# Kernel tuning notes

Hardware: AMD Instinct MI355X
Metric: run time of the kernel (lower is better)

The kernel has to match this reference:

```python
import jax, jax.numpy as jnp
import numpy as np

N = 50000
E = 800000
D = 512
H = 256
K = 16
COLLAPSE_REG = 1.0


def setup_inputs() -> dict:
    key = jax.random.key(0)
    ks = jax.random.split(key, 8)
    embeddings = jax.random.normal(ks[0], (N, D), dtype=jnp.float32)
    edge_src = jax.random.randint(ks[1], (E,), 0, N, dtype=jnp.int32)
    edge_dst = jax.random.randint(ks[2], (E,), 0, N, dtype=jnp.int32)
    # GCNConv params (glorot-ish scaling)
    W1 = jax.random.normal(ks[3], (D, H), dtype=jnp.float32) / np.sqrt(D)
    b1 = jnp.zeros((H,), dtype=jnp.float32)
    W2 = jax.random.normal(ks[4], (H, H), dtype=jnp.float32) / np.sqrt(H)
    b2 = jnp.zeros((H,), dtype=jnp.float32)
    Wa = jax.random.normal(ks[5], (H, K), dtype=jnp.float32) / np.sqrt(H)
    ba = jnp.zeros((K,), dtype=jnp.float32)
    return {"embeddings": embeddings, "edge_src": edge_src, "edge_dst": edge_dst,
            "W1": W1, "b1": b1, "W2": W2, "b2": b2, "Wa": Wa, "ba": ba}


def _gcn_conv(x, W, b, src, dst, dis):
    # PyG GCNConv: transform then D^{-1/2}(A+I)D^{-1/2} aggregation + bias.
    x = x @ W                                   # [N, out]
    norm = dis[src] * dis[dst]                  # [E]
    agg = jax.ops.segment_sum(x[src] * norm[:, None], dst, num_segments=N)
    agg = agg + (dis * dis)[:, None] * x        # self-loop term
    return agg + b


def reference(embeddings, edge_src, edge_dst, W1, b1, W2, b2, Wa, ba):
    # symmetric-norm degrees with self-loops (edge weight 1)
    deg = 1.0 + jax.ops.segment_sum(jnp.ones((E,), jnp.float32), edge_dst, num_segments=N)
    dis = jax.lax.rsqrt(deg)                    # deg > 0 always (self-loop)

    x = jax.nn.selu(_gcn_conv(embeddings, W1, b1, edge_src, edge_dst, dis))
    x_skip = x  # dropout is identity in eval
    x = jax.nn.selu(_gcn_conv(x, W2, b2, edge_src, edge_dst, dis))
    x = x + x_skip
    assignments = jax.nn.softmax(x @ Wa + ba, axis=1)   # [N, K]

    # ---- DMoN losses (faithful to original, incl. scalar normalizer) ----
    degrees = jax.ops.segment_sum(jnp.ones((E,), jnp.float32), edge_src, num_segments=N)  # row sums of A
    m = degrees.sum() / 2.0
    AS = jax.ops.segment_sum(assignments[edge_dst], edge_src, num_segments=N)  # A @ S, [N, K]
    trace_pooled = jnp.sum(assignments * AS)    # trace(S^T A S)
    dS = degrees @ assignments                  # [K]
    normalizer = jnp.dot(dS, dS) / (2.0 * m)    # scalar (as in original code)
    spectral_loss = -(trace_pooled - K * normalizer) / (2.0 * m)

    cluster_sizes = assignments.sum(axis=0)     # [K]
    collapse_loss = jnp.linalg.norm(cluster_sizes) / N * jnp.sqrt(jnp.float32(K)) - 1.0
    entropy = -jnp.sum(assignments * jnp.log(assignments + 1e-8)) / N
    entropy_loss = -0.1 * entropy
    total_loss = spectral_loss + COLLAPSE_REG * collapse_loss + entropy_loss

    pooled = (assignments / (cluster_sizes + 1e-8)).T @ embeddings  # [K, D]
    return (assignments, pooled, spectral_loss, COLLAPSE_REG * collapse_loss, total_loss, entropy_loss)
```

## Files before the change

kernel.cpp:

```cpp
#include <hip/hip_runtime.h>
#include <hip/hip_fp16.h>
#include <math.h>

#define NN 50000
#define EE 800000
#define DD 512
#define HH 256
#define KK 16
#define NB_SCAN 196

typedef _Float16 half8_t __attribute__((ext_vector_type(8)));
typedef float f32x4 __attribute__((ext_vector_type(4)));

__global__ void zero_kernel(int* __restrict__ p, int n) {
    int i = blockIdx.x * blockDim.x + threadIdx.x;
    if (i < n) p[i] = 0;
}

__global__ void count_kernel(const int4* __restrict__ src4, const int4* __restrict__ dst4,
                             int* __restrict__ indeg, int* __restrict__ outdeg) {
    int e = blockIdx.x * blockDim.x + threadIdx.x;
    if (e < EE / 4) {
        int4 s = src4[e], d = dst4[e];
        atomicAdd(&outdeg[s.x], 1); atomicAdd(&outdeg[s.y], 1);
        atomicAdd(&outdeg[s.z], 1); atomicAdd(&outdeg[s.w], 1);
        atomicAdd(&indeg[d.x], 1);  atomicAdd(&indeg[d.y], 1);
        atomicAdd(&indeg[d.z], 1);  atomicAdd(&indeg[d.w], 1);
    }
}

__global__ void scan_p1(const int* __restrict__ in, int* __restrict__ part, int n,
                        const int* __restrict__ outdeg, float* __restrict__ dis,
                        float* __restrict__ degf) {
    __shared__ int tile[256];
    int t = threadIdx.x;
    int i = blockIdx.x * 256 + t;
    int v = (i < n) ? in[i] : 0;
    tile[t] = v;
    if (i < n) {
        dis[i]  = 1.0f / sqrtf(1.0f + (float)v);
        degf[i] = (float)outdeg[i];
    }
    __syncthreads();
    for (int o = 128; o > 0; o >>= 1) {
        if (t < o) tile[t] += tile[t + o];
        __syncthreads();
    }
    if (t == 0) part[blockIdx.x] = tile[0];
}

__global__ void scan_p2(int* __restrict__ part, int nb, int* __restrict__ off_end) {
    __shared__ int tile[256];
    int t = threadIdx.x;
    int v = (t < nb) ? part[t] : 0;
    tile[t] = v;
    __syncthreads();
    for (int o = 1; o < 256; o <<= 1) {
        int x = (t >= o) ? tile[t - o] : 0;
        __syncthreads();
        tile[t] += x;
        __syncthreads();
    }
    if (t < nb) part[t] = tile[t] - v;
    if (t == 255) *off_end = tile[255];
}

__global__ void scan_p3(const int* __restrict__ in, const int* __restrict__ part,
                        int* __restrict__ out, int n) {
    __shared__ int tile[256];
    int t = threadIdx.x;
    int i = blockIdx.x * 256 + t;
    int v = (i < n) ? in[i] : 0;
    tile[t] = v;
    __syncthreads();
    for (int o = 1; o < 256; o <<= 1) {
        int x = (t >= o) ? tile[t - o] : 0;
        __syncthreads();
        tile[t] += x;
        __syncthreads();
    }
    if (i < n) out[i] = part[blockIdx.x] + tile[t] - v;
}

__global__ void scatter_kernel(const int4* __restrict__ src4, const int4* __restrict__ dst4,
                               const int* __restrict__ off, int* __restrict__ cur,
                               int* __restrict__ nbr) {
    int e = blockIdx.x * blockDim.x + threadIdx.x;
    if (e < EE / 4) {
        int4 s = src4[e], d = dst4[e];
        int p;
        p = atomicAdd(&cur[d.x], 1); nbr[off[d.x] + p] = s.x;
        p = atomicAdd(&cur[d.y], 1); nbr[off[d.y] + p] = s.y;
        p = atomicAdd(&cur[d.z], 1); nbr[off[d.z] + p] = s.z;
        p = atomicAdd(&cur[d.w], 1); nbr[off[d.w] + p] = s.w;
    }
}

__global__ void transpose_w(const float* __restrict__ W1, __half* __restrict__ Wt1,
                            const float* __restrict__ W2, __half* __restrict__ Wt2,
                            const float* __restrict__ Wa, __half* __restrict__ WaT) {
    int i = blockIdx.x * 256 + threadIdx.x;
    if (i < DD * HH) {
        int k = i / HH, n = i % HH;
        Wt1[(size_t)n * DD + k] = __float2half(W1[i]);
    } else if (i < DD * HH + HH * HH) {
        int j = i - DD * HH;
        int k = j / HH, n = j % HH;
        Wt2[(size_t)n * HH + k] = __float2half(W2[j]);
    } else if (i < DD * HH + HH * HH + HH * KK) {
        int j = i - DD * HH - HH * HH;
        int k = j / KK, n = j % KK;
        WaT[n * HH + k] = __float2half(Wa[j]);
    }
}

template <typename TA, int KDIM>
__global__ __launch_bounds__(256) void mfma_gemm(const TA* __restrict__ A,
                                                 const __half* __restrict__ Bt,
                                                 __half* __restrict__ C, int M) {
    constexpr bool F32 = sizeof(TA) == 4;
    constexpr int SROW = F32 ? 36 : 40;
    constexpr int EPG  = F32 ? 4 : 8;
    constexpr int GPR  = 32 / EPG;
    constexpr int RPP  = 256 / GPR;
    constexpr int NP   = 128 / RPP;
    constexpr int KI   = KDIM / 32;

    __shared__ TA As[2][128 * SROW];

    int t = threadIdx.x;
    int wave = t >> 6, lane = t & 63, quad = lane >> 4, l16 = lane & 15;
    int row0 = blockIdx.x * 128, col0 = blockIdx.y * 128;
    int wm = (wave & 1) * 64, wn = (wave >> 1) * 64;
    int srow = t / GPR, sg = t % GPR;

    f32x4 acc[4][4] = {};
    uint4 sreg[NP];
    uint4 bcur[4];

    const __half* brow[4];
#pragma unroll
    for (int ni = 0; ni < 4; ni++)
        brow[ni] = Bt + (size_t)(col0 + wn + ni * 16 + l16) * KDIM + quad * 8;

    auto gloadA = [&](int k0) {
#pragma unroll
        for (int p = 0; p < NP; p++) {
            int gr = row0 + p * RPP + srow;
            if (gr < M)
                sreg[p] = *(const uint4*)(A + (size_t)gr * KDIM + k0 + sg * EPG);
            else
                sreg[p] = make_uint4(0, 0, 0, 0);
        }
    };
    auto sstore = [&](int buf) {
#pragma unroll
        for (int p = 0; p < NP; p++)
            *(uint4*)&As[buf][(p * RPP + srow) * SROW + sg * EPG] = sreg[p];
    };

    gloadA(0);
#pragma unroll
    for (int ni = 0; ni < 4; ni++) bcur[ni] = *(const uint4*)(brow[ni]);
    sstore(0);
    __syncthreads();

#pragma unroll
    for (int i = 0; i < KI; i++) {
        int cur = i & 1;
        uint4 bnext[4];
        if (i + 1 < KI) {
            gloadA((i + 1) * 32);
#pragma unroll
            for (int ni = 0; ni < 4; ni++)
                bnext[ni] = *(const uint4*)(brow[ni] + (i + 1) * 32);
        }

        half8_t af[4];
#pragma unroll
        for (int mi = 0; mi < 4; mi++) {
            int row = wm + mi * 16 + l16;
            if constexpr (F32) {
                const float* pl = (const float*)&As[cur][0] + row * SROW + quad * 8;
                float4 x0 = *(const float4*)pl;
                float4 x1 = *(const float4*)(pl + 4);
                half8_t h;
                h[0] = (_Float16)x0.x; h[1] = (_Float16)x0.y;
                h[2] = (_Float16)x0.z; h[3] = (_Float16)x0.w;
                h[4] = (_Float16)x1.x; h[5] = (_Float16)x1.y;
                h[6] = (_Float16)x1.z; h[7] = (_Float16)x1.w;
                af[mi] = h;
            } else {
                af[mi] = *(const half8_t*)&As[cur][row * SROW + quad * 8];
            }
        }
#pragma unroll
        for (int mi = 0; mi < 4; mi++)
#pragma unroll
            for (int ni = 0; ni < 4; ni++)
                acc[mi][ni] = __builtin_amdgcn_mfma_f32_16x16x32_f16(
                    af[mi], *(half8_t*)&bcur[ni], acc[mi][ni], 0, 0, 0);

        if (i + 1 < KI) {
            sstore(cur ^ 1);
#pragma unroll
            for (int ni = 0; ni < 4; ni++) bcur[ni] = bnext[ni];
        }
        __syncthreads();
    }

#pragma unroll
    for (int mi = 0; mi < 4; mi++) {
#pragma unroll
        for (int r = 0; r < 4; r++) {
            int rr = row0 + wm + mi * 16 + quad * 4 + r;
            if (rr < M) {
#pragma unroll
                for (int ni = 0; ni < 4; ni++) {
                    C[(size_t)rr * HH + col0 + wn + ni * 16 + l16] =
                        __float2half(acc[mi][ni][r]);
                }
            }
        }
    }
}

__device__ inline void fma8(float* acc, uint4 raw, float w) {
    const __half2* h = (const __half2*)&raw;
#pragma unroll
    for (int i = 0; i < 4; i++) {
        float2 f = __half22float2(h[i]);
        acc[2 * i]     += w * f.x;
        acc[2 * i + 1] += w * f.y;
    }
}

__global__ __launch_bounds__(256) void agg_selu(const __half* __restrict__ T,
                                                const float* __restrict__ dis,
                                                const int* __restrict__ off,
                                                const int* __restrict__ nbr,
                                                const float* __restrict__ bias,
                                                const __half* skip, __half* out) {
    int t = threadIdx.x;
    int l32 = t & 31;
    int n = blockIdx.x * 8 + (t >> 5);
    int c = l32 * 8;
    float dn = dis[n];

    float acc[8];
#pragma unroll
    for (int i = 0; i < 8; i++) acc[i] = 0.f;
    fma8(acc, *(const uint4*)(T + (size_t)n * HH + c), dn * dn);

    int s0 = off[n], s1 = off[n + 1];
    for (int base = s0; base < s1; base += 32) {
        int cnt = min(32, s1 - base);
        int sidv = 0; float sdsv = 0.f;
        if (l32 < cnt) {
            sidv = nbr[base + l32];
            sdsv = dis[sidv] * dn;
        }
        int j = 0;
        for (; j + 8 <= cnt; j += 8) {
            int a0 = __shfl(sidv, j, 32),     a1 = __shfl(sidv, j + 1, 32);
            int a2 = __shfl(sidv, j + 2, 32), a3 = __shfl(sidv, j + 3, 32);
            int a4 = __shfl(sidv, j + 4, 32), a5 = __shfl(sidv, j + 5, 32);
            int a6 = __shfl(sidv, j + 6, 32), a7 = __shfl(sidv, j + 7, 32);
            float w0 = __shfl(sdsv, j, 32),     w1 = __shfl(sdsv, j + 1, 32);
            float w2 = __shfl(sdsv, j + 2, 32), w3 = __shfl(sdsv, j + 3, 32);
            float w4 = __shfl(sdsv, j + 4, 32), w5 = __shfl(sdsv, j + 5, 32);
            float w6 = __shfl(sdsv, j + 6, 32), w7 = __shfl(sdsv, j + 7, 32);
            uint4 r0 = *(const uint4*)(T + (size_t)a0 * HH + c);
            uint4 r1 = *(const uint4*)(T + (size_t)a1 * HH + c);
            uint4 r2 = *(const uint4*)(T + (size_t)a2 * HH + c);
            uint4 r3 = *(const uint4*)(T + (size_t)a3 * HH + c);
            uint4 r4 = *(const uint4*)(T + (size_t)a4 * HH + c);
            uint4 r5 = *(const uint4*)(T + (size_t)a5 * HH + c);
            uint4 r6 = *(const uint4*)(T + (size_t)a6 * HH + c);
            uint4 r7 = *(const uint4*)(T + (size_t)a7 * HH + c);
            fma8(acc, r0, w0); fma8(acc, r1, w1);
            fma8(acc, r2, w2); fma8(acc, r3, w3);
            fma8(acc, r4, w4); fma8(acc, r5, w5);
            fma8(acc, r6, w6); fma8(acc, r7, w7);
        }
        for (; j < cnt; j++) {
            int s = __shfl(sidv, j, 32);
            float w = __shfl(sdsv, j, 32);
            fma8(acc, *(const uint4*)(T + (size_t)s * HH + c), w);
        }
    }

    const float scale = 1.0507009873554805f;
    const float alpha = 1.6732632423543772f;
    float4 b0 = *(const float4*)(bias + c);
    float4 b1 = *(const float4*)(bias + c + 4);
    float bb[8] = {b0.x, b0.y, b0.z, b0.w, b1.x, b1.y, b1.z, b1.w};
    float sk8[8];
#pragma unroll
    for (int i = 0; i < 8; i++) sk8[i] = 0.f;
    if (skip) {
        uint4 raw = *(const uint4*)(skip + (size_t)n * HH + c);
        const __half2* h = (const __half2*)&raw;
#pragma unroll
        for (int i = 0; i < 4; i++) {
            float2 f = __half22float2(h[i]);
            sk8[2 * i] = f.x; sk8[2 * i + 1] = f.y;
        }
    }
    _Float16 res[8];
#pragma unroll
    for (int i = 0; i < 8; i++) {
        float v = acc[i] + bb[i];
        float r = v > 0.f ? scale * v : scale * alpha * expm1f(v);
        res[i] = (_Float16)(r + sk8[i]);
    }
    *(uint4*)(out + (size_t)n * HH + c) = *(uint4*)res;
}

__global__ __launch_bounds__(256) void assign_mfma(const __half* __restrict__ Hb,
                                                   const __half* __restrict__ WaT,
                                                   const float* __restrict__ ba,
                                                   const float* __restrict__ degf,
                                                   float* __restrict__ out_assign,
                                                   __half* __restrict__ out_f16,
                                                   float* __restrict__ scal) {
    int t = threadIdx.x;
    int wave = t >> 6, lane = t & 63, quad = lane >> 4, l16 = lane & 15;
    int nb = blockIdx.x * 256 + wave * 64;

    f32x4 acc[4] = {};
    const __half* bp = WaT + l16 * HH + quad * 8;
    const __half* ap[4];
#pragma unroll
    for (int mi = 0; mi < 4; mi++) {
        int r = nb + mi * 16 + l16;
        if (r >= NN) r = NN - 1;
        ap[mi] = Hb + (size_t)r * HH + quad * 8;
    }
#pragma unroll
    for (int s = 0; s < 8; s++) {
        half8_t bf = *(const half8_t*)(bp + s * 32);
#pragma unroll
        for (int mi = 0; mi < 4; mi++) {
            half8_t af = *(const half8_t*)(ap[mi] + s * 32);
            acc[mi] = __builtin_amdgcn_mfma_f32_16x16x32_f16(af, bf, acc[mi], 0, 0, 0);
        }
    }

    float myb = ba[l16];
    float lcs = 0.f, ldS = 0.f, lent = 0.f;
#pragma unroll
    for (int mi = 0; mi < 4; mi++) {
#pragma unroll
        for (int r = 0; r < 4; r++) {
            int node = nb + mi * 16 + quad * 4 + r;
            bool ok = node < NN;
            float logit = acc[mi][r] + myb;
            float mx = logit;
            for (int o = 1; o < 16; o <<= 1) mx = fmaxf(mx, __shfl_xor(mx, o, 16));
            float e = expf(logit - mx);
            float sum = e;
            for (int o = 1; o < 16; o <<= 1) sum += __shfl_xor(sum, o, 16);
            float a = e / sum;
            if (ok) {
                out_assign[(size_t)node * KK + l16] = a;
                out_f16[(size_t)node * KK + l16] = __float2half(a);
                lcs += a;
                ldS += degf[node] * a;
                lent += a * logf(a + 1e-8f);
            }
        }
    }
    lcs += __shfl_xor(lcs, 16); lcs += __shfl_xor(lcs, 32);
    ldS += __shfl_xor(ldS, 16); ldS += __shfl_xor(ldS, 32);
    for (int o = 32; o >= 1; o >>= 1) lent += __shfl_xor(lent, o);
    if (quad == 0) {
        atomicAdd(&scal[l16], lcs);
        atomicAdd(&scal[16 + l16], ldS);
    }
    if (lane == 0) atomicAdd(&scal[33], lent);
}

__device__ inline float dot16h(const __half* a, const __half* b) {
    uint4 a0 = *(const uint4*)a, a1 = *(const uint4*)(a + 8);
    uint4 b0 = *(const uint4*)b, b1 = *(const uint4*)(b + 8);
    float p = 0.f;
    const __half2* xa = (const __half2*)&a0;
    const __half2* xb = (const __half2*)&b0;
#pragma unroll
    for (int i = 0; i < 4; i++) {
        float2 u = __half22float2(xa[i]), v = __half22float2(xb[i]);
        p += u.x * v.x + u.y * v.y;
    }
    xa = (const __half2*)&a1; xb = (const __half2*)&b1;
#pragma unroll
    for (int i = 0; i < 4; i++) {
        float2 u = __half22float2(xa[i]), v = __half22float2(xb[i]);
        p += u.x * v.x + u.y * v.y;
    }
    return p;
}

__global__ __launch_bounds__(256) void edge_trace(const int4* __restrict__ src4,
                                                  const int4* __restrict__ dst4,
                                                  const __half* __restrict__ Ah,
                                                  float* __restrict__ scal) {
    int e = blockIdx.x * blockDim.x + threadIdx.x;
    float p = 0.f;
    if (e < EE / 4) {
        int4 s = src4[e], d = dst4[e];
        p += dot16h(Ah + (size_t)s.x * KK, Ah + (size_t)d.x * KK);
        p += dot16h(Ah + (size_t)s.y * KK, Ah + (size_t)d.y * KK);
        p += dot16h(Ah + (size_t)s.z * KK, Ah + (size_t)d.z * KK);
        p += dot16h(Ah + (size_t)s.w * KK, Ah + (size_t)d.w * KK);
    }
    for (int o = 32; o >= 1; o >>= 1) p += __shfl_xor(p, o);
    __shared__ float sp;
    if (threadIdx.x == 0) sp = 0.f;
    __syncthreads();
    if ((threadIdx.x & 63) == 0) atomicAdd(&sp, p);
    __syncthreads();
    if (threadIdx.x == 0) atomicAdd(&scal[32], sp);
}

#define PCH 125
__global__ __launch_bounds__(256) void pooled_partial(const float* __restrict__ emb,
                                                      const float* __restrict__ assign,
                                                      float* __restrict__ pool_acc) {
    int d = blockIdx.x * 256 + threadIdx.x;
    int c0 = blockIdx.y * PCH;
    float acc[KK];
#pragma unroll
    for (int k = 0; k < KK; k++) acc[k] = 0.f;
    __shared__ float sa[PCH * KK];
    {
        const float4* srcv = (const float4*)(assign + (size_t)c0 * KK);
        float4* dstv = (float4*)sa;
        for (int i = threadIdx.x; i < PCH * KK / 4; i += 256) dstv[i] = srcv[i];
    }
    __syncthreads();
    for (int j = 0; j < PCH; j++) {
        float ev = emb[(size_t)(c0 + j) * DD + d];
#pragma unroll
        for (int k4 = 0; k4 < 4; k4++) {
            float4 s4 = *(const float4*)&sa[j * KK + k4 * 4];
            acc[k4 * 4 + 0] += s4.x * ev;
            acc[k4 * 4 + 1] += s4.y * ev;
            acc[k4 * 4 + 2] += s4.z * ev;
            acc[k4 * 4 + 3] += s4.w * ev;
        }
    }
#pragma unroll
    for (int k = 0; k < KK; k++) atomicAdd(&pool_acc[k * DD + d], acc[k]);
}

__global__ void finalize(const float* __restrict__ pool_acc, const float* __restrict__ scal,
                         float* __restrict__ out) {
    int bx = blockIdx.x, t = threadIdx.x;
    if (bx < 32) {
        int i = bx * 256 + t;
        int k = i / DD;
        out[800000 + i] = pool_acc[i] / (scal[k] + 1e-8f);
    } else if (t == 0) {
        float cs2 = 0.f, ds2 = 0.f;
        for (int k = 0; k < KK; k++) {
            cs2 += scal[k] * scal[k];
            ds2 += scal[16 + k] * scal[16 + k];
        }
        float two_m = (float)EE;
        float normalizer = ds2 / two_m;
        float trace = scal[32];
        float spectral = -(trace - (float)KK * normalizer) / two_m;
        float collapse = sqrtf(cs2) / (float)NN * 4.0f - 1.0f;
        float entl = 0.1f * scal[33] / (float)NN;
        out[808192] = spectral;
        out[808193] = collapse;
        out[808194] = spectral + collapse + entl;
        out[808195] = entl;
    }
}

extern "C" void kernel_launch(void* const* d_in, const int* in_sizes, int n_in,
                              void* d_out, int out_size, void* d_ws, size_t ws_size,
                              hipStream_t stream) {
    const float* emb = (const float*)d_in[0];
    const int* esrc  = (const int*)d_in[1];
    const int* edst  = (const int*)d_in[2];
    const float* W1  = (const float*)d_in[3];
    const float* b1  = (const float*)d_in[4];
    const float* W2  = (const float*)d_in[5];
    const float* b2  = (const float*)d_in[6];
    const float* Wa  = (const float*)d_in[7];
    const float* ba  = (const float*)d_in[8];
    float* out = (float*)d_out;

    int* indeg      = (int*)d_ws;
    int* outdeg     = indeg + 50000;
    int* cur        = outdeg + 50000;
    float* pool_acc = (float*)(cur + 50000);
    float* scal     = pool_acc + 8192;
    int* part       = (int*)(scal + 64);
    int* off        = part + 256;
    int* nbr        = off + 50004;
    float* dis      = (float*)(nbr + 800000);
    float* degf     = dis + 50000;
    __half* Wt1     = (__half*)(degf + 50000);
    __half* Wt2     = Wt1 + 256 * 512;
    __half* WaT     = Wt2 + 256 * 256;
    __half* T       = WaT + 16 * 256;
    __half* Hb      = T + (size_t)NN * HH;
    __half* Ah      = T;

    zero_kernel<<<dim3(619), 256, 0, stream>>>((int*)d_ws, 158256);
    count_kernel<<<dim3(782), 256, 0, stream>>>((const int4*)esrc, (const int4*)edst,
                                                indeg, outdeg);

    scan_p1<<<dim3(NB_SCAN), 256, 0, stream>>>(indeg, part, NN, outdeg, dis, degf);
    scan_p2<<<dim3(1), 256, 0, stream>>>(part, NB_SCAN, off + NN);
    scan_p3<<<dim3(NB_SCAN), 256, 0, stream>>>(indeg, part, off, NN);
    scatter_kernel<<<dim3(782), 256, 0, stream>>>((const int4*)esrc, (const int4*)edst,
                                                  off, cur, nbr);

    transpose_w<<<dim3(784), 256, 0, stream>>>(W1, Wt1, W2, Wt2, Wa, WaT);

    mfma_gemm<float, DD><<<dim3(392, 2), 256, 0, stream>>>(emb, Wt1, T, NN);
    agg_selu<<<dim3(6250), 256, 0, stream>>>(T, dis, off, nbr, b1, nullptr, Hb);

    mfma_gemm<__half, HH><<<dim3(392, 2), 256, 0, stream>>>(Hb, Wt2, T, NN);
    agg_selu<<<dim3(6250), 256, 0, stream>>>(T, dis, off, nbr, b2, Hb, Hb);

    assign_mfma<<<dim3(196), 256, 0, stream>>>(Hb, WaT, ba, degf, out, Ah, scal);
    edge_trace<<<dim3(782), 256, 0, stream>>>((const int4*)esrc, (const int4*)edst, Ah, scal);
    pooled_partial<<<dim3(2, 400), 256, 0, stream>>>(emb, out, pool_acc);
    finalize<<<dim3(33), 256, 0, stream>>>(pool_acc, scal, out);
}
```

Measured before the change: 563.8 us.

## Slice GEMM output into column panels and precompute edge weights for aggregation

```diff
diff --git a/kernel.cpp b/kernel.cpp
--- a/kernel.cpp
+++ b/kernel.cpp
@@ -84,15 +84,20 @@
 
 __global__ void scatter_kernel(const int4* __restrict__ src4, const int4* __restrict__ dst4,
                                const int* __restrict__ off, int* __restrict__ cur,
-                               int* __restrict__ nbr) {
+                               const float* __restrict__ dis,
+                               int* __restrict__ nbr, __half* __restrict__ wgt) {
     int e = blockIdx.x * blockDim.x + threadIdx.x;
     if (e < EE / 4) {
         int4 s = src4[e], d = dst4[e];
-        int p;
-        p = atomicAdd(&cur[d.x], 1); nbr[off[d.x] + p] = s.x;
-        p = atomicAdd(&cur[d.y], 1); nbr[off[d.y] + p] = s.y;
-        p = atomicAdd(&cur[d.z], 1); nbr[off[d.z] + p] = s.z;
-        p = atomicAdd(&cur[d.w], 1); nbr[off[d.w] + p] = s.w;
+        int p, q;
+        p = atomicAdd(&cur[d.x], 1); q = off[d.x] + p;
+        nbr[q] = s.x; wgt[q] = __float2half(dis[s.x] * dis[d.x]);
+        p = atomicAdd(&cur[d.y], 1); q = off[d.y] + p;
+        nbr[q] = s.y; wgt[q] = __float2half(dis[s.y] * dis[d.y]);
+        p = atomicAdd(&cur[d.z], 1); q = off[d.z] + p;
+        nbr[q] = s.z; wgt[q] = __float2half(dis[s.z] * dis[d.z]);
+        p = atomicAdd(&cur[d.w], 1); q = off[d.w] + p;
+        nbr[q] = s.w; wgt[q] = __float2half(dis[s.w] * dis[d.w]);
     }
 }
 
@@ -217,7 +222,8 @@
             if (rr < M) {
 #pragma unroll
                 for (int ni = 0; ni < 4; ni++) {
-                    C[(size_t)rr * HH + col0 + wn + ni * 16 + l16] =
+                    int c = col0 + wn + ni * 16 + l16;
+                    C[((size_t)(c >> 5) * NN + rr) * 32 + (c & 31)] =
                         __float2half(acc[mi][ni][r]);
                 }
             }
@@ -235,71 +241,75 @@
     }
 }
 
-__global__ __launch_bounds__(256) void agg_selu(const __half* __restrict__ T,
+__global__ __launch_bounds__(256) void agg_selu(const __half* __restrict__ Ts,
                                                 const float* __restrict__ dis,
                                                 const int* __restrict__ off,
                                                 const int* __restrict__ nbr,
+                                                const __half* __restrict__ wgt,
                                                 const float* __restrict__ bias,
                                                 const __half* skip, __half* out) {
     int t = threadIdx.x;
-    int l32 = t & 31;
-    int n = blockIdx.x * 8 + (t >> 5);
-    int c = l32 * 8;
+    int s = blockIdx.x & 7;
+    int n = (blockIdx.x >> 3) * 64 + (t >> 2);
+    if (n >= NN) return;
+    int l4 = t & 3;
+    int c4 = l4 * 8;
+    const __half* Tsl = Ts + (size_t)s * NN * 32;
     float dn = dis[n];
 
     float acc[8];
 #pragma unroll
     for (int i = 0; i < 8; i++) acc[i] = 0.f;
-    fma8(acc, *(const uint4*)(T + (size_t)n * HH + c), dn * dn);
+    fma8(acc, *(const uint4*)(Tsl + (size_t)n * 32 + c4), dn * dn);
 
     int s0 = off[n], s1 = off[n + 1];
-    for (int base = s0; base < s1; base += 32) {
-        int cnt = min(32, s1 - base);
-        int sidv = 0; float sdsv = 0.f;
-        if (l32 < cnt) {
-            sidv = nbr[base + l32];
-            sdsv = dis[sidv] * dn;
-        }
-        int j = 0;
-        for (; j + 8 <= cnt; j += 8) {
-            int a0 = __shfl(sidv, j, 32),     a1 = __shfl(sidv, j + 1, 32);
-            int a2 = __shfl(sidv, j + 2, 32), a3 = __shfl(sidv, j + 3, 32);
-            int a4 = __shfl(sidv, j + 4, 32), a5 = __shfl(sidv, j + 5, 32);
-            int a6 = __shfl(sidv, j + 6, 32), a7 = __shfl(sidv, j + 7, 32);
-            float w0 = __shfl(sdsv, j, 32),     w1 = __shfl(sdsv, j + 1, 32);
-            float w2 = __shfl(sdsv, j + 2, 32), w3 = __shfl(sdsv, j + 3, 32);
-            float w4 = __shfl(sdsv, j + 4, 32), w5 = __shfl(sdsv, j + 5, 32);
-            float w6 = __shfl(sdsv, j + 6, 32), w7 = __shfl(sdsv, j + 7, 32);
-            uint4 r0 = *(const uint4*)(T + (size_t)a0 * HH + c);
-            uint4 r1 = *(const uint4*)(T + (size_t)a1 * HH + c);
-            uint4 r2 = *(const uint4*)(T + (size_t)a2 * HH + c);
-            uint4 r3 = *(const uint4*)(T + (size_t)a3 * HH + c);
-            uint4 r4 = *(const uint4*)(T + (size_t)a4 * HH + c);
-            uint4 r5 = *(const uint4*)(T + (size_t)a5 * HH + c);
-            uint4 r6 = *(const uint4*)(T + (size_t)a6 * HH + c);
-            uint4 r7 = *(const uint4*)(T + (size_t)a7 * HH + c);
-            fma8(acc, r0, w0); fma8(acc, r1, w1);
-            fma8(acc, r2, w2); fma8(acc, r3, w3);
-            fma8(acc, r4, w4); fma8(acc, r5, w5);
-            fma8(acc, r6, w6); fma8(acc, r7, w7);
-        }
-        for (; j < cnt; j++) {
-            int s = __shfl(sidv, j, 32);
-            float w = __shfl(sdsv, j, 32);
-            fma8(acc, *(const uint4*)(T + (size_t)s * HH + c), w);
+    int base = s0;
+    for (; base + 8 <= s1; base += 8) {
+        int i0 = __builtin_nontemporal_load(&nbr[base + l4]);
+        int i1 = __builtin_nontemporal_load(&nbr[base + 4 + l4]);
+        unsigned short u0 = __builtin_nontemporal_load((const unsigned short*)&wgt[base + l4]);
+        unsigned short u1 = __builtin_nontemporal_load((const unsigned short*)&wgt[base + 4 + l4]);
+        __half h0 = *(__half*)&u0, h1 = *(__half*)&u1;
+        float w0f = __half2float(h0), w1f = __half2float(h1);
+        int id[8]; float ww[8];
+#pragma unroll
+        for (int j = 0; j < 4; j++) {
+            id[j]     = __shfl(i0, j, 4); ww[j]     = __shfl(w0f, j, 4);
+            id[4 + j] = __shfl(i1, j, 4); ww[4 + j] = __shfl(w1f, j, 4);
+        }
+        uint4 r[8];
+#pragma unroll
+        for (int j = 0; j < 8; j++)
+            r[j] = *(const uint4*)(Tsl + (size_t)id[j] * 32 + c4);
+#pragma unroll
+        for (int j = 0; j < 8; j++) fma8(acc, r[j], ww[j]);
+    }
+    for (; base < s1; base += 4) {
+        int cnt = min(4, s1 - base);
+        int iv = 0; float wv = 0.f;
+        if (l4 < cnt) {
+            iv = __builtin_nontemporal_load(&nbr[base + l4]);
+            unsigned short u = __builtin_nontemporal_load((const unsigned short*)&wgt[base + l4]);
+            wv = __half2float(*(__half*)&u);
+        }
+        for (int j = 0; j < cnt; j++) {
+            int idx = __shfl(iv, j, 4);
+            float w = __shfl(wv, j, 4);
+            fma8(acc, *(const uint4*)(Tsl + (size_t)idx * 32 + c4), w);
         }
     }
 
     const float scale = 1.0507009873554805f;
     const float alpha = 1.6732632423543772f;
-    float4 b0 = *(const float4*)(bias + c);
-    float4 b1 = *(const float4*)(bias + c + 4);
+    int cg = s * 32 + c4;
+    float4 b0 = *(const float4*)(bias + cg);
+    float4 b1 = *(const float4*)(bias + cg + 4);
     float bb[8] = {b0.x, b0.y, b0.z, b0.w, b1.x, b1.y, b1.z, b1.w};
     float sk8[8];
 #pragma unroll
     for (int i = 0; i < 8; i++) sk8[i] = 0.f;
     if (skip) {
-        uint4 raw = *(const uint4*)(skip + (size_t)n * HH + c);
+        uint4 raw = *(const uint4*)(skip + (size_t)n * HH + cg);
         const __half2* h = (const __half2*)&raw;
 #pragma unroll
         for (int i = 0; i < 4; i++) {
@@ -314,7 +324,7 @@
         float r = v > 0.f ? scale * v : scale * alpha * expm1f(v);
         res[i] = (_Float16)(r + sk8[i]);
     }
-    *(uint4*)(out + (size_t)n * HH + c) = *(uint4*)res;
+    *(uint4*)(out + (size_t)n * HH + cg) = *(uint4*)res;
 }
 
 __global__ __launch_bounds__(256) void assign_mfma(const __half* __restrict__ Hb,
@@ -504,7 +514,8 @@
     int* nbr        = off + 50004;
     float* dis      = (float*)(nbr + 800000);
     float* degf     = dis + 50000;
-    __half* Wt1     = (__half*)(degf + 50000);
+    __half* wgt     = (__half*)(degf + 50000);
+    __half* Wt1     = wgt + 800000;
     __half* Wt2     = Wt1 + 256 * 512;
     __half* WaT     = Wt2 + 256 * 256;
     __half* T       = WaT + 16 * 256;
@@ -519,15 +530,15 @@
     scan_p2<<<dim3(1), 256, 0, stream>>>(part, NB_SCAN, off + NN);
     scan_p3<<<dim3(NB_SCAN), 256, 0, stream>>>(indeg, part, off, NN);
     scatter_kernel<<<dim3(782), 256, 0, stream>>>((const int4*)esrc, (const int4*)edst,
-                                                  off, cur, nbr);
+                                                  off, cur, dis, nbr, wgt);
 
     transpose_w<<<dim3(784), 256, 0, stream>>>(W1, Wt1, W2, Wt2, Wa, WaT);
 
     mfma_gemm<float, DD><<<dim3(392, 2), 256, 0, stream>>>(emb, Wt1, T, NN);
-    agg_selu<<<dim3(6250), 256, 0, stream>>>(T, dis, off, nbr, b1, nullptr, Hb);
+    agg_selu<<<dim3(6256), 256, 0, stream>>>(T, dis, off, nbr, wgt, b1, nullptr, Hb);
 
     mfma_gemm<__half, HH><<<dim3(392, 2), 256, 0, stream>>>(Hb, Wt2, T, NN);
-    agg_selu<<<dim3(6250), 256, 0, stream>>>(T, dis, off, nbr, b2, Hb, Hb);
+    agg_selu<<<dim3(6256), 256, 0, stream>>>(T, dis, off, nbr, wgt, b2, Hb, Hb);
 
     assign_mfma<<<dim3(196), 256, 0, stream>>>(Hb, WaT, ba, degf, out, Ah, scal);
     edge_trace<<<dim3(782), 256, 0, stream>>>((const int4*)esrc, (const int4*)edst, Ah, scal);
```

New measurement: 662.8 us. 17.6% more time.

## Load GEMM fragments directly from global and precompute per-edge fp16 weights

Applied to the files above, without the earlier changes.

```diff
diff --git a/kernel.cpp b/kernel.cpp
--- a/kernel.cpp
+++ b/kernel.cpp
@@ -84,15 +84,20 @@
 
 __global__ void scatter_kernel(const int4* __restrict__ src4, const int4* __restrict__ dst4,
                                const int* __restrict__ off, int* __restrict__ cur,
-                               int* __restrict__ nbr) {
+                               const float* __restrict__ dis,
+                               int* __restrict__ nbr, __half* __restrict__ wgt) {
     int e = blockIdx.x * blockDim.x + threadIdx.x;
     if (e < EE / 4) {
         int4 s = src4[e], d = dst4[e];
-        int p;
-        p = atomicAdd(&cur[d.x], 1); nbr[off[d.x] + p] = s.x;
-        p = atomicAdd(&cur[d.y], 1); nbr[off[d.y] + p] = s.y;
-        p = atomicAdd(&cur[d.z], 1); nbr[off[d.z] + p] = s.z;
-        p = atomicAdd(&cur[d.w], 1); nbr[off[d.w] + p] = s.w;
+        int p, q;
+        p = atomicAdd(&cur[d.x], 1); q = off[d.x] + p;
+        nbr[q] = s.x; wgt[q] = __float2half(dis[s.x] * dis[d.x]);
+        p = atomicAdd(&cur[d.y], 1); q = off[d.y] + p;
+        nbr[q] = s.y; wgt[q] = __float2half(dis[s.y] * dis[d.y]);
+        p = atomicAdd(&cur[d.z], 1); q = off[d.z] + p;
+        nbr[q] = s.z; wgt[q] = __float2half(dis[s.z] * dis[d.z]);
+        p = atomicAdd(&cur[d.w], 1); q = off[d.w] + p;
+        nbr[q] = s.w; wgt[q] = __float2half(dis[s.w] * dis[d.w]);
     }
 }
 
@@ -114,99 +119,67 @@
     }
 }
 
+__device__ inline half8_t loadfrag(const float* p) {
+    float4 x0 = *(const float4*)p;
+    float4 x1 = *(const float4*)(p + 4);
+    half8_t h;
+    h[0] = (_Float16)x0.x; h[1] = (_Float16)x0.y;
+    h[2] = (_Float16)x0.z; h[3] = (_Float16)x0.w;
+    h[4] = (_Float16)x1.x; h[5] = (_Float16)x1.y;
+    h[6] = (_Float16)x1.z; h[7] = (_Float16)x1.w;
+    return h;
+}
+__device__ inline half8_t loadfrag(const __half* p) { return *(const half8_t*)p; }
+
 template <typename TA, int KDIM>
 __global__ __launch_bounds__(256) void mfma_gemm(const TA* __restrict__ A,
                                                  const __half* __restrict__ Bt,
                                                  __half* __restrict__ C, int M) {
-    constexpr bool F32 = sizeof(TA) == 4;
-    constexpr int SROW = F32 ? 36 : 40;
-    constexpr int EPG  = F32 ? 4 : 8;
-    constexpr int GPR  = 32 / EPG;
-    constexpr int RPP  = 256 / GPR;
-    constexpr int NP   = 128 / RPP;
-    constexpr int KI   = KDIM / 32;
-
-    __shared__ TA As[2][128 * SROW];
-
+    constexpr int KI = KDIM / 32;
     int t = threadIdx.x;
     int wave = t >> 6, lane = t & 63, quad = lane >> 4, l16 = lane & 15;
     int row0 = blockIdx.x * 128, col0 = blockIdx.y * 128;
     int wm = (wave & 1) * 64, wn = (wave >> 1) * 64;
-    int srow = t / GPR, sg = t % GPR;
+
+    const TA* ap[4];
+    const __half* bp[4];
+#pragma unroll
+    for (int mi = 0; mi < 4; mi++) {
+        int r = row0 + wm + mi * 16 + l16;
+        if (r >= M) r = M - 1;
+        ap[mi] = A + (size_t)r * KDIM + quad * 8;
+    }
+#pragma unroll
+    for (int ni = 0; ni < 4; ni++)
+        bp[ni] = Bt + (size_t)(col0 + wn + ni * 16 + l16) * KDIM + quad * 8;
 
     f32x4 acc[4][4] = {};
-    uint4 sreg[NP];
-    uint4 bcur[4];
-
-    const __half* brow[4];
-#pragma unroll
-    for (int ni = 0; ni < 4; ni++)
-        brow[ni] = Bt + (size_t)(col0 + wn + ni * 16 + l16) * KDIM + quad * 8;
-
-    auto gloadA = [&](int k0) {
-#pragma unroll
-        for (int p = 0; p < NP; p++) {
-            int gr = row0 + p * RPP + srow;
-            if (gr < M)
-                sreg[p] = *(const uint4*)(A + (size_t)gr * KDIM + k0 + sg * EPG);
-            else
-                sreg[p] = make_uint4(0, 0, 0, 0);
-        }
-    };
-    auto sstore = [&](int buf) {
-#pragma unroll
-        for (int p = 0; p < NP; p++)
-            *(uint4*)&As[buf][(p * RPP + srow) * SROW + sg * EPG] = sreg[p];
-    };
-
-    gloadA(0);
-#pragma unroll
-    for (int ni = 0; ni < 4; ni++) bcur[ni] = *(const uint4*)(brow[ni]);
-    sstore(0);
-    __syncthreads();
+    half8_t af[4], bf[4], afn[4], bfn[4];
+#pragma unroll
+    for (int mi = 0; mi < 4; mi++) af[mi] = loadfrag(ap[mi]);
+#pragma unroll
+    for (int ni = 0; ni < 4; ni++) bf[ni] = loadfrag(bp[ni]);
 
 #pragma unroll
     for (int i = 0; i < KI; i++) {
-        int cur = i & 1;
-        uint4 bnext[4];
         if (i + 1 < KI) {
-            gloadA((i + 1) * 32);
-#pragma unroll
-            for (int ni = 0; ni < 4; ni++)
-                bnext[ni] = *(const uint4*)(brow[ni] + (i + 1) * 32);
-        }
-
-        half8_t af[4];
-#pragma unroll
-        for (int mi = 0; mi < 4; mi++) {
-            int row = wm + mi * 16 + l16;
-            if constexpr (F32) {
-                const float* pl = (const float*)&As[cur][0] + row * SROW + quad * 8;
-                float4 x0 = *(const float4*)pl;
-                float4 x1 = *(const float4*)(pl + 4);
-                half8_t h;
-                h[0] = (_Float16)x0.x; h[1] = (_Float16)x0.y;
-                h[2] = (_Float16)x0.z; h[3] = (_Float16)x0.w;
-                h[4] = (_Float16)x1.x; h[5] = (_Float16)x1.y;
-                h[6] = (_Float16)x1.z; h[7] = (_Float16)x1.w;
-                af[mi] = h;
-            } else {
-                af[mi] = *(const half8_t*)&As[cur][row * SROW + quad * 8];
-            }
+#pragma unroll
+            for (int mi = 0; mi < 4; mi++) afn[mi] = loadfrag(ap[mi] + (i + 1) * 32);
+#pragma unroll
+            for (int ni = 0; ni < 4; ni++) bfn[ni] = loadfrag(bp[ni] + (i + 1) * 32);
         }
 #pragma unroll
         for (int mi = 0; mi < 4; mi++)
 #pragma unroll
             for (int ni = 0; ni < 4; ni++)
                 acc[mi][ni] = __builtin_amdgcn_mfma_f32_16x16x32_f16(
-                    af[mi], *(half8_t*)&bcur[ni], acc[mi][ni], 0, 0, 0);
-
+                    af[mi], bf[ni], acc[mi][ni], 0, 0, 0);
         if (i + 1 < KI) {
-            sstore(cur ^ 1);
-#pragma unroll
-            for (int ni = 0; ni < 4; ni++) bcur[ni] = bnext[ni];
-        }
-        __syncthreads();
+#pragma unroll
+            for (int mi = 0; mi < 4; mi++) af[mi] = afn[mi];
+#pragma unroll
+            for (int ni = 0; ni < 4; ni++) bf[ni] = bfn[ni];
+        }
     }
 
 #pragma unroll
@@ -239,6 +212,7 @@
                                                 const float* __restrict__ dis,
                                                 const int* __restrict__ off,
                                                 const int* __restrict__ nbr,
+                                                const __half* __restrict__ wgt,
                                                 const float* __restrict__ bias,
                                                 const __half* skip, __half* out) {
     int t = threadIdx.x;
@@ -255,10 +229,10 @@
     int s0 = off[n], s1 = off[n + 1];
     for (int base = s0; base < s1; base += 32) {
         int cnt = min(32, s1 - base);
-        int sidv = 0; float sdsv = 0.f;
+        int sidv = 0; float wv = 0.f;
         if (l32 < cnt) {
             sidv = nbr[base + l32];
-            sdsv = dis[sidv] * dn;
+            wv = __half2float(wgt[base + l32]);
         }
         int j = 0;
         for (; j + 8 <= cnt; j += 8) {
@@ -266,10 +240,10 @@
             int a2 = __shfl(sidv, j + 2, 32), a3 = __shfl(sidv, j + 3, 32);
             int a4 = __shfl(sidv, j + 4, 32), a5 = __shfl(sidv, j + 5, 32);
             int a6 = __shfl(sidv, j + 6, 32), a7 = __shfl(sidv, j + 7, 32);
-            float w0 = __shfl(sdsv, j, 32),     w1 = __shfl(sdsv, j + 1, 32);
-            float w2 = __shfl(sdsv, j + 2, 32), w3 = __shfl(sdsv, j + 3, 32);
-            float w4 = __shfl(sdsv, j + 4, 32), w5 = __shfl(sdsv, j + 5, 32);
-            float w6 = __shfl(sdsv, j + 6, 32), w7 = __shfl(sdsv, j + 7, 32);
+            float w0 = __shfl(wv, j, 32),     w1 = __shfl(wv, j + 1, 32);
+            float w2 = __shfl(wv, j + 2, 32), w3 = __shfl(wv, j + 3, 32);
+            float w4 = __shfl(wv, j + 4, 32), w5 = __shfl(wv, j + 5, 32);
+            float w6 = __shfl(wv, j + 6, 32), w7 = __shfl(wv, j + 7, 32);
             uint4 r0 = *(const uint4*)(T + (size_t)a0 * HH + c);
             uint4 r1 = *(const uint4*)(T + (size_t)a1 * HH + c);
             uint4 r2 = *(const uint4*)(T + (size_t)a2 * HH + c);
@@ -285,7 +259,7 @@
         }
         for (; j < cnt; j++) {
             int s = __shfl(sidv, j, 32);
-            float w = __shfl(sdsv, j, 32);
+            float w = __shfl(wv, j, 32);
             fma8(acc, *(const uint4*)(T + (size_t)s * HH + c), w);
         }
     }
@@ -504,7 +478,8 @@
     int* nbr        = off + 50004;
     float* dis      = (float*)(nbr + 800000);
     float* degf     = dis + 50000;
-    __half* Wt1     = (__half*)(degf + 50000);
+    __half* wgt     = (__half*)(degf + 50000);
+    __half* Wt1     = wgt + 800000;
     __half* Wt2     = Wt1 + 256 * 512;
     __half* WaT     = Wt2 + 256 * 256;
     __half* T       = WaT + 16 * 256;
@@ -519,15 +494,15 @@
     scan_p2<<<dim3(1), 256, 0, stream>>>(part, NB_SCAN, off + NN);
     scan_p3<<<dim3(NB_SCAN), 256, 0, stream>>>(indeg, part, off, NN);
     scatter_kernel<<<dim3(782), 256, 0, stream>>>((const int4*)esrc, (const int4*)edst,
-                                                  off, cur, nbr);
+                                                  off, cur, dis, nbr, wgt);
 
     transpose_w<<<dim3(784), 256, 0, stream>>>(W1, Wt1, W2, Wt2, Wa, WaT);
 
     mfma_gemm<float, DD><<<dim3(392, 2), 256, 0, stream>>>(emb, Wt1, T, NN);
-    agg_selu<<<dim3(6250), 256, 0, stream>>>(T, dis, off, nbr, b1, nullptr, Hb);
+    agg_selu<<<dim3(6250), 256, 0, stream>>>(T, dis, off, nbr, wgt, b1, nullptr, Hb);
 
     mfma_gemm<__half, HH><<<dim3(392, 2), 256, 0, stream>>>(Hb, Wt2, T, NN);
-    agg_selu<<<dim3(6250), 256, 0, stream>>>(T, dis, off, nbr, b2, Hb, Hb);
+    agg_selu<<<dim3(6250), 256, 0, stream>>>(T, dis, off, nbr, wgt, b2, Hb, Hb);
 
     assign_mfma<<<dim3(196), 256, 0, stream>>>(Hb, WaT, ba, degf, out, Ah, scal);
     edge_trace<<<dim3(782), 256, 0, stream>>>((const int4*)esrc, (const int4*)edst, Ah, scal);
```

After: 618.1 us. +9.6%, slower.
